# Performance work log

Measured on AMD Instinct MI355X. Metric: run time of the kernel, lower is better.

The kernel has to match this reference:

```python
import jax, jax.numpy as jnp
import numpy as np

GRID_SIZE = 32
GRID_BOUND = 0.5


def point_closest_cell_index(points):
    grid_min = -GRID_BOUND + GRID_BOUND / GRID_SIZE
    inds = (points - grid_min) * GRID_SIZE / (2.0 * GRID_BOUND)
    return jnp.round(jnp.clip(inds, 0.0, GRID_SIZE - 1))


def cal_distance(trans_points, cp, voxel, weight=1.0):
    # trans_points: [B,N,3], cp: [B,G^3,3], voxel: [B,G^3] (0/1 occupancy)
    nb = point_closest_cell_index(trans_points)  # [B,N,3]
    strides = jnp.array([GRID_SIZE ** 2, GRID_SIZE, 1], dtype=trans_points.dtype)
    idx = (nb @ strides).astype(jnp.int32)  # [B,N] flattened voxel index
    mask = 1.0 - jnp.take_along_axis(voxel, idx, axis=1)  # [B,N]
    closest = jnp.take_along_axis(cp, idx[..., None], axis=1)  # [B,N,3]
    d = (trans_points - closest) * mask[..., None]
    return jnp.mean(jnp.sum(d * d, axis=(1, 2))) * weight


def plane_sym_transform(points, p):
    # reflect points across plane n.x + d = 0; p = [nx,ny,nz,d]
    n, d = p[:3], p[3]
    dist = (points @ n + d) / jnp.sum(n * n)
    return points - 2.0 * dist[..., None] * n


def rot_sym_transform(points, q):
    # rotate points by (normalized) quaternion q = [w,x,y,z]
    q = q / jnp.sqrt(jnp.sum(q * q))
    w, u = q[0], q[1:]
    t = 2.0 * jnp.cross(jnp.broadcast_to(u, points.shape), points)
    return points + w * t + jnp.cross(jnp.broadcast_to(u, t.shape), t)


def setup_inputs() -> dict:
    key = jax.random.key(0)
    ks = jax.random.split(key, 5)
    B, N, G3 = 256, 4096, GRID_SIZE ** 3
    points = jax.random.normal(ks[0], (B, N, 3), jnp.float32) * 0.25
    cp = jax.random.normal(ks[1], (B, G3, 3), jnp.float32) * 0.25
    voxel = (jax.random.uniform(ks[2], (B, G3), jnp.float32) < 0.2).astype(jnp.float32)
    plane = jax.random.normal(ks[3], (3, 4), jnp.float32)
    quat = jax.random.normal(ks[4], (3, 4), jnp.float32)
    return {"points": points, "cp": cp, "voxel": voxel, "plane": plane, "quat": quat}


def reference(points, cp, voxel, plane, quat):
    ref_loss = jnp.zeros((1,), points.dtype)
    rot_loss = jnp.zeros((1,), points.dtype)
    for i in range(plane.shape[0]):
        ref_points = plane_sym_transform(points, plane[i])
        ref_loss = ref_loss + cal_distance(ref_points, cp, voxel)
    for i in range(quat.shape[0]):
        rot_points = rot_sym_transform(points, quat[i])
        rot_loss = rot_loss + cal_distance(rot_points, cp, voxel)
    return ref_loss, rot_loss
```

## Files before the change

### kernel.cpp

```cpp
#include <hip/hip_runtime.h>

#define G3 32768
#define SLABS 4
#define SLAB_CELLS 8192
#define TPB 1024

__global__ __launch_bounds__(TPB)
void symloss_slab_kernel(const float* __restrict__ points,
                         const float* __restrict__ cp,
                         const float* __restrict__ voxel,
                         const float* __restrict__ plane,
                         const float* __restrict__ quat,
                         float* __restrict__ out,
                         int N, float invB)
{
    __shared__ float4 slab[SLAB_CELLS];
    __shared__ float sR[TPB / 64], sQ[TPB / 64];

    const int row  = blockIdx.x >> 2;
    const int base = (blockIdx.x & 3) * SLAB_CELLS;

    const float* __restrict__ cpb  = cp     + (size_t)row * (G3 * 3);
    const float* __restrict__ voxb = voxel  + (size_t)row * G3;
    const float* __restrict__ ptb  = points + (size_t)row * (size_t)N * 3;

    float pnx[3], pny[3], pnz[3], pdd[3], pinv[3];
    float qw[3], qux[3], quy[3], quz[3];
#pragma unroll
    for (int i = 0; i < 3; ++i) {
        float nx = plane[4*i+0], ny = plane[4*i+1], nz = plane[4*i+2], dd = plane[4*i+3];
        pnx[i] = nx; pny[i] = ny; pnz[i] = nz; pdd[i] = dd;
        pinv[i] = 1.0f / (nx*nx + ny*ny + nz*nz);

        float w  = quat[4*i+0], ux = quat[4*i+1], uy = quat[4*i+2], uz = quat[4*i+3];
        float rn = 1.0f / sqrtf(w*w + ux*ux + uy*uy + uz*uz);
        qw[i] = w*rn; qux[i] = ux*rn; quy[i] = uy*rn; quz[i] = uz*rn;
    }

#pragma unroll
    for (int c = threadIdx.x; c < SLAB_CELLS; c += TPB) {
        int g = base + c;
        float4 v;
        v.x = __builtin_nontemporal_load(&cpb[3*g+0]);
        v.y = __builtin_nontemporal_load(&cpb[3*g+1]);
        v.z = __builtin_nontemporal_load(&cpb[3*g+2]);
        v.w = 1.0f - __builtin_nontemporal_load(&voxb[g]);
        slab[c] = v;
    }
    __syncthreads();

    const float gmin = -0.484375f;

    float accR = 0.0f, accQ = 0.0f;

    for (int p = threadIdx.x; p < N; p += TPB) {
        float px = ptb[3*p+0];
        float py = ptb[3*p+1];
        float pz = ptb[3*p+2];

#pragma unroll
        for (int t = 0; t < 3; ++t) {
            float dist = (px*pnx[t] + py*pny[t] + pz*pnz[t] + pdd[t]) * pinv[t];
            float rx = px - 2.0f * dist * pnx[t];
            float ry = py - 2.0f * dist * pny[t];
            float rz = pz - 2.0f * dist * pnz[t];
            {
                float fx = rintf(fminf(fmaxf((rx - gmin) * 32.0f, 0.0f), 31.0f));
                float fy = rintf(fminf(fmaxf((ry - gmin) * 32.0f, 0.0f), 31.0f));
                float fz = rintf(fminf(fmaxf((rz - gmin) * 32.0f, 0.0f), 31.0f));
                int local = (int)(fx * 1024.0f + fy * 32.0f + fz) - base;
                if ((unsigned)local < SLAB_CELLS) {
                    float4 c4 = slab[local];
                    float dx = (rx - c4.x) * c4.w;
                    float dy = (ry - c4.y) * c4.w;
                    float dz = (rz - c4.z) * c4.w;
                    accR += dx*dx + dy*dy + dz*dz;
                }
            }

            float tx = 2.0f * (quy[t]*pz - quz[t]*py);
            float ty = 2.0f * (quz[t]*px - qux[t]*pz);
            float tz = 2.0f * (qux[t]*py - quy[t]*px);
            float ox = px + qw[t]*tx + (quy[t]*tz - quz[t]*ty);
            float oy = py + qw[t]*ty + (quz[t]*tx - qux[t]*tz);
            float oz = pz + qw[t]*tz + (qux[t]*ty - quy[t]*tx);
            {
                float fx = rintf(fminf(fmaxf((ox - gmin) * 32.0f, 0.0f), 31.0f));
                float fy = rintf(fminf(fmaxf((oy - gmin) * 32.0f, 0.0f), 31.0f));
                float fz = rintf(fminf(fmaxf((oz - gmin) * 32.0f, 0.0f), 31.0f));
                int local = (int)(fx * 1024.0f + fy * 32.0f + fz) - base;
                if ((unsigned)local < SLAB_CELLS) {
                    float4 c4 = slab[local];
                    float dx = (ox - c4.x) * c4.w;
                    float dy = (oy - c4.y) * c4.w;
                    float dz = (oz - c4.z) * c4.w;
                    accQ += dx*dx + dy*dy + dz*dz;
                }
            }
        }
    }

#pragma unroll
    for (int off = 32; off > 0; off >>= 1) {
        accR += __shfl_down(accR, off, 64);
        accQ += __shfl_down(accQ, off, 64);
    }
    int wave = threadIdx.x >> 6;
    int lane = threadIdx.x & 63;
    if (lane == 0) { sR[wave] = accR; sQ[wave] = accQ; }
    __syncthreads();
    if (threadIdx.x == 0) {
        float r = 0.0f, q = 0.0f;
#pragma unroll
        for (int w = 0; w < TPB / 64; ++w) { r += sR[w]; q += sQ[w]; }
        atomicAdd(&out[0], r * invB);
        atomicAdd(&out[1], q * invB);
    }
}

extern "C" void kernel_launch(void* const* d_in, const int* in_sizes, int n_in,
                              void* d_out, int out_size, void* d_ws, size_t ws_size,
                              hipStream_t stream)
{
    const float* points = (const float*)d_in[0];
    const float* cp     = (const float*)d_in[1];
    const float* voxel  = (const float*)d_in[2];
    const float* plane  = (const float*)d_in[3];
    const float* quat   = (const float*)d_in[4];
    float* out = (float*)d_out;

    int B = in_sizes[2] / G3;
    int N = (in_sizes[0] / 3) / B;
    float invB = 1.0f / (float)B;

    hipMemsetAsync(out, 0, (size_t)out_size * sizeof(float), stream);

    symloss_slab_kernel<<<B * SLABS, TPB, 0, stream>>>(points, cp, voxel, plane, quat,
                                                       out, N, invB);
}
```

Measured before the change: 214.0 us.

## Pack voxel slab as fp16 to halve slabs per row, vectorize loads

The closest-point/mask slab in LDS is now stored as four packed fp16 values (8 bytes per cell) instead of a float4. That fits 16384 cells per block, so each batch row needs 2 blocks instead of 4 and the points are re-read and re-transformed half as often. Global loads of cp, voxel and points are vectorized to float4, and each thread prefetches its first point group before the slab fill. The change adds fp16 rounding error to the closest-point coordinates, which may shift the loss slightly.

```diff
diff --git a/kernel.cpp b/kernel.cpp
--- a/kernel.cpp
+++ b/kernel.cpp
@@ -1,9 +1,71 @@
 #include <hip/hip_runtime.h>
+#include <hip/hip_fp16.h>
 
 #define G3 32768
-#define SLABS 4
-#define SLAB_CELLS 8192
+#define SLABS 2
+#define SLAB_CELLS 16384
 #define TPB 1024
+
+typedef float f32x4 __attribute__((ext_vector_type(4)));
+
+static __device__ __forceinline__ unsigned pack2h(float a, float b) {
+    unsigned short ua = __half_as_ushort(__float2half(a));
+    unsigned short ub = __half_as_ushort(__float2half(b));
+    return (unsigned)ua | ((unsigned)ub << 16);
+}
+static __device__ __forceinline__ float lo2f(unsigned u) {
+    return __half2float(__ushort_as_half((unsigned short)(u & 0xffffu)));
+}
+static __device__ __forceinline__ float hi2f(unsigned u) {
+    return __half2float(__ushort_as_half((unsigned short)(u >> 16)));
+}
+
+#define PROCESS(PX, PY, PZ, ACCR_EXPR, ACCQ_EXPR)                                   \
+    do {                                                                            \
+        _Pragma("unroll")                                                           \
+        for (int t = 0; t < 3; ++t) {                                               \
+                                        \
+            float dist = ((PX)*pnx[t] + (PY)*pny[t] + (PZ)*pnz[t] + pdd[t]) * pinv[t]; \
+            float rx = (PX) - 2.0f * dist * pnx[t];                                 \
+            float ry = (PY) - 2.0f * dist * pny[t];                                 \
+            float rz = (PZ) - 2.0f * dist * pnz[t];                                 \
+            {                                                                       \
+                float fx = rintf(fminf(fmaxf((rx - gmin) * 32.0f, 0.0f), 31.0f));   \
+                float fy = rintf(fminf(fmaxf((ry - gmin) * 32.0f, 0.0f), 31.0f));   \
+                float fz = rintf(fminf(fmaxf((rz - gmin) * 32.0f, 0.0f), 31.0f));   \
+                int local = (int)(fx * 1024.0f + fy * 32.0f + fz) - base;           \
+                if ((unsigned)local < SLAB_CELLS) {                                 \
+                    uint2 u = slab[local];                                          \
+                    float m  = hi2f(u.y);                                           \
+                    float dx = (rx - lo2f(u.x)) * m;                                \
+                    float dy = (ry - hi2f(u.x)) * m;                                \
+                    float dz = (rz - lo2f(u.y)) * m;                                \
+                    ACCR_EXPR += dx*dx + dy*dy + dz*dz;                             \
+                }                                                                   \
+            }                                                                       \
+                                     \
+            float tx = 2.0f * (quy[t]*(PZ) - quz[t]*(PY));                          \
+            float ty = 2.0f * (quz[t]*(PX) - qux[t]*(PZ));                          \
+            float tz = 2.0f * (qux[t]*(PY) - quy[t]*(PX));                          \
+            float ox = (PX) + qw[t]*tx + (quy[t]*tz - quz[t]*ty);                   \
+            float oy = (PY) + qw[t]*ty + (quz[t]*tx - qux[t]*tz);                   \
+            float oz = (PZ) + qw[t]*tz + (qux[t]*ty - quy[t]*tx);                   \
+            {                                                                       \
+                float fx = rintf(fminf(fmaxf((ox - gmin) * 32.0f, 0.0f), 31.0f));   \
+                float fy = rintf(fminf(fmaxf((oy - gmin) * 32.0f, 0.0f), 31.0f));   \
+                float fz = rintf(fminf(fmaxf((oz - gmin) * 32.0f, 0.0f), 31.0f));   \
+                int local = (int)(fx * 1024.0f + fy * 32.0f + fz) - base;           \
+                if ((unsigned)local < SLAB_CELLS) {                                 \
+                    uint2 u = slab[local];                                          \
+                    float m  = hi2f(u.y);                                           \
+                    float dx = (ox - lo2f(u.x)) * m;                                \
+                    float dy = (oy - hi2f(u.x)) * m;                                \
+                    float dz = (oz - lo2f(u.y)) * m;                                \
+                    ACCQ_EXPR += dx*dx + dy*dy + dz*dz;                             \
+                }                                                                   \
+            }                                                                       \
+        }                                                                           \
+    } while (0)
 
 __global__ __launch_bounds__(TPB)
 void symloss_slab_kernel(const float* __restrict__ points,
@@ -14,15 +76,25 @@
                          float* __restrict__ out,
                          int N, float invB)
 {
-    __shared__ float4 slab[SLAB_CELLS];
+    __shared__ uint2 slab[SLAB_CELLS];
     __shared__ float sR[TPB / 64], sQ[TPB / 64];
 
-    const int row  = blockIdx.x >> 2;
-    const int base = (blockIdx.x & 3) * SLAB_CELLS;
+    const int row  = blockIdx.x >> 1;
+    const int base = (blockIdx.x & 1) * SLAB_CELLS;
 
-    const float* __restrict__ cpb  = cp     + (size_t)row * (G3 * 3);
-    const float* __restrict__ voxb = voxel  + (size_t)row * G3;
+    const float* __restrict__ cpb  = cp     + (size_t)row * (G3 * 3) + (size_t)base * 3;
+    const float* __restrict__ voxb = voxel  + (size_t)row * G3 + base;
     const float* __restrict__ ptb  = points + (size_t)row * (size_t)N * 3;
+
+    const float4* __restrict__ pt4 = reinterpret_cast<const float4*>(ptb);
+    const int ngrp = N >> 2;
+    float4 q0, q1, q2;
+    const bool havePts = (int)threadIdx.x < ngrp;
+    if (havePts) {
+        q0 = pt4[3 * threadIdx.x + 0];
+        q1 = pt4[3 * threadIdx.x + 1];
+        q2 = pt4[3 * threadIdx.x + 2];
+    }
 
     float pnx[3], pny[3], pnz[3], pdd[3], pinv[3];
     float qw[3], qux[3], quy[3], quz[3];
@@ -37,67 +109,38 @@
         qw[i] = w*rn; qux[i] = ux*rn; quy[i] = uy*rn; quz[i] = uz*rn;
     }
 
-#pragma unroll
-    for (int c = threadIdx.x; c < SLAB_CELLS; c += TPB) {
-        int g = base + c;
-        float4 v;
-        v.x = __builtin_nontemporal_load(&cpb[3*g+0]);
-        v.y = __builtin_nontemporal_load(&cpb[3*g+1]);
-        v.z = __builtin_nontemporal_load(&cpb[3*g+2]);
-        v.w = 1.0f - __builtin_nontemporal_load(&voxb[g]);
-        slab[c] = v;
+    const f32x4* __restrict__ cp4 = reinterpret_cast<const f32x4*>(cpb);
+    const f32x4* __restrict__ vx4 = reinterpret_cast<const f32x4*>(voxb);
+#pragma unroll 2
+    for (int gI = threadIdx.x; gI < SLAB_CELLS / 4; gI += TPB) {
+        f32x4 v0 = __builtin_nontemporal_load(&cp4[3*gI+0]);
+        f32x4 v1 = __builtin_nontemporal_load(&cp4[3*gI+1]);
+        f32x4 v2 = __builtin_nontemporal_load(&cp4[3*gI+2]);
+        f32x4 w  = __builtin_nontemporal_load(&vx4[gI]);
+        uint2 c0; c0.x = pack2h(v0.x, v0.y); c0.y = pack2h(v0.z, 1.0f - w.x);
+        uint2 c1; c1.x = pack2h(v0.w, v1.x); c1.y = pack2h(v1.y, 1.0f - w.y);
+        uint2 c2; c2.x = pack2h(v1.z, v1.w); c2.y = pack2h(v2.x, 1.0f - w.z);
+        uint2 c3; c3.x = pack2h(v2.y, v2.z); c3.y = pack2h(v2.w, 1.0f - w.w);
+        slab[4*gI+0] = c0; slab[4*gI+1] = c1;
+        slab[4*gI+2] = c2; slab[4*gI+3] = c3;
     }
     __syncthreads();
 
     const float gmin = -0.484375f;
-
     float accR = 0.0f, accQ = 0.0f;
 
-    for (int p = threadIdx.x; p < N; p += TPB) {
-        float px = ptb[3*p+0];
-        float py = ptb[3*p+1];
-        float pz = ptb[3*p+2];
-
-#pragma unroll
-        for (int t = 0; t < 3; ++t) {
-            float dist = (px*pnx[t] + py*pny[t] + pz*pnz[t] + pdd[t]) * pinv[t];
-            float rx = px - 2.0f * dist * pnx[t];
-            float ry = py - 2.0f * dist * pny[t];
-            float rz = pz - 2.0f * dist * pnz[t];
-            {
-                float fx = rintf(fminf(fmaxf((rx - gmin) * 32.0f, 0.0f), 31.0f));
-                float fy = rintf(fminf(fmaxf((ry - gmin) * 32.0f, 0.0f), 31.0f));
-                float fz = rintf(fminf(fmaxf((rz - gmin) * 32.0f, 0.0f), 31.0f));
-                int local = (int)(fx * 1024.0f + fy * 32.0f + fz) - base;
-                if ((unsigned)local < SLAB_CELLS) {
-                    float4 c4 = slab[local];
-                    float dx = (rx - c4.x) * c4.w;
-                    float dy = (ry - c4.y) * c4.w;
-                    float dz = (rz - c4.z) * c4.w;
-                    accR += dx*dx + dy*dy + dz*dz;
-                }
-            }
-
-            float tx = 2.0f * (quy[t]*pz - quz[t]*py);
-            float ty = 2.0f * (quz[t]*px - qux[t]*pz);
-            float tz = 2.0f * (qux[t]*py - quy[t]*px);
-            float ox = px + qw[t]*tx + (quy[t]*tz - quz[t]*ty);
-            float oy = py + qw[t]*ty + (quz[t]*tx - qux[t]*tz);
-            float oz = pz + qw[t]*tz + (qux[t]*ty - quy[t]*tx);
-            {
-                float fx = rintf(fminf(fmaxf((ox - gmin) * 32.0f, 0.0f), 31.0f));
-                float fy = rintf(fminf(fmaxf((oy - gmin) * 32.0f, 0.0f), 31.0f));
-                float fz = rintf(fminf(fmaxf((oz - gmin) * 32.0f, 0.0f), 31.0f));
-                int local = (int)(fx * 1024.0f + fy * 32.0f + fz) - base;
-                if ((unsigned)local < SLAB_CELLS) {
-                    float4 c4 = slab[local];
-                    float dx = (ox - c4.x) * c4.w;
-                    float dy = (oy - c4.y) * c4.w;
-                    float dz = (oz - c4.z) * c4.w;
-                    accQ += dx*dx + dy*dy + dz*dz;
-                }
-            }
-        }
+    if (havePts) {
+        PROCESS(q0.x, q0.y, q0.z, accR, accQ);
+        PROCESS(q0.w, q1.x, q1.y, accR, accQ);
+        PROCESS(q1.z, q1.w, q2.x, accR, accQ);
+        PROCESS(q2.y, q2.z, q2.w, accR, accQ);
+    }
+    for (int g4 = threadIdx.x + TPB; g4 < ngrp; g4 += TPB) {
+        float4 a0 = pt4[3*g4+0], a1 = pt4[3*g4+1], a2 = pt4[3*g4+2];
+        PROCESS(a0.x, a0.y, a0.z, accR, accQ);
+        PROCESS(a0.w, a1.x, a1.y, accR, accQ);
+        PROCESS(a1.z, a1.w, a2.x, accR, accQ);
+        PROCESS(a2.y, a2.z, a2.w, accR, accQ);
     }
 
 #pragma unroll
@@ -133,7 +176,7 @@
     int N = (in_sizes[0] / 3) / B;
     float invB = 1.0f / (float)B;
 
-    hipMemsetAsync(out, 0, (size_t)out_size * sizeof(float), stream);
+    (void)hipMemsetAsync(out, 0, (size_t)out_size * sizeof(float), stream);
 
     symloss_slab_kernel<<<B * SLABS, TPB, 0, stream>>>(points, cp, voxel, plane, quat,
                                                        out, N, invB);
```

Result: faster. 207.1 us (-3.2%).
